# Kernel tuning notes

Measured on AMD Instinct MI355X. Metric: run time of the kernel, lower is better.

Reference implementation:

```python
import jax, jax.numpy as jnp
import numpy as np

# Config: 4 sparse batch items, each with 2048 active voxels (uniform-length case
# of sparse full self-attention). channels=1024, heads=16, head_dim=64.
B_SEQ, L, H, D = 4, 2048, 16, 64
C = H * D  # 1024
N = B_SEQ * L  # 8192
EPS = 1e-12  # F.normalize eps


def setup_inputs() -> dict:
    key = jax.random.key(0)
    ks = jax.random.split(key, 6)
    s = 1.0 / np.sqrt(C)
    return {
        "x": jax.random.normal(ks[0], (N, C), dtype=jnp.float32),
        "W_qkv": jax.random.normal(ks[1], (C, 3 * C), dtype=jnp.float32) * s,
        "b_qkv": jnp.zeros((3 * C,), dtype=jnp.float32),
        "gamma_q": jnp.ones((H, D), dtype=jnp.float32),
        "gamma_k": jnp.ones((H, D), dtype=jnp.float32),
        "W_out": jax.random.normal(ks[2], (C, C), dtype=jnp.float32) * s,
        "b_out": jnp.zeros((C,), dtype=jnp.float32),
    }


def _qk_rms_norm(t, gamma):
    # SparseMultiHeadRMSNorm: L2-normalize last dim, scale by gamma[h,d] * sqrt(D)
    norm = jnp.maximum(jnp.linalg.norm(t, axis=-1, keepdims=True), EPS)
    return (t / norm) * gamma * (D ** 0.5)


def reference(x, W_qkv, b_qkv, gamma_q, gamma_k, W_out, b_out):
    qkv = x @ W_qkv + b_qkv                       # [N, 3C]
    qkv = qkv.reshape(B_SEQ, L, 3, H, D)          # fused pre-reshape
    q, k, v = qkv[:, :, 0], qkv[:, :, 1], qkv[:, :, 2]  # [B,L,H,D]
    q = _qk_rms_norm(q, gamma_q)
    k = _qk_rms_norm(k, gamma_k)
    # full scaled dot-product attention within each sparse batch item
    scores = jnp.einsum('blhd,bmhd->bhlm', q, k) / (D ** 0.5)
    attn = jax.nn.softmax(scores, axis=-1)
    h = jnp.einsum('bhlm,bmhd->blhd', attn, v)    # [B,L,H,D]
    h = h.reshape(N, C)
    return h @ W_out + b_out
```

## Files before the change

kernel.cpp:

```cpp
#include <hip/hip_runtime.h>

using u16 = unsigned short;

typedef float  f32x4  __attribute__((ext_vector_type(4)));
typedef float  f32x16 __attribute__((ext_vector_type(16)));
typedef __bf16 bf16x8 __attribute__((ext_vector_type(8)));
typedef short  s16x8  __attribute__((ext_vector_type(8)));

#define DEVI __device__ __forceinline__

constexpr int TOK = 8192;
constexpr int CIN = 1024;
constexpr int C3  = 3072;
constexpr int NH  = 16;
constexpr int HD  = 64;
constexpr int SL  = 2048;
constexpr int BH  = 64;

constexpr float LOG2E = 1.4426950408889634f;

DEVI u16 f2bf(float x) {
  unsigned u = __builtin_bit_cast(unsigned, x);
  u += 0x7FFFu + ((u >> 16) & 1u);
  return (u16)(u >> 16);
}

DEVI f32x4 mfma16(s16x8 a, s16x8 b, f32x4 c) {
  return __builtin_amdgcn_mfma_f32_16x16x32_bf16(
      __builtin_bit_cast(bf16x8, a), __builtin_bit_cast(bf16x8, b), c, 0, 0, 0);
}

DEVI f32x16 mfma32(s16x8 a, s16x8 b, f32x16 c) {
  return __builtin_amdgcn_mfma_f32_32x32x16_bf16(
      __builtin_bit_cast(bf16x8, a), __builtin_bit_cast(bf16x8, b), c, 0, 0, 0);
}

DEVI void gload_lds16(const void* g, void* l) {
  __builtin_amdgcn_global_load_lds(
      (const __attribute__((address_space(1))) unsigned int*)g,
      (__attribute__((address_space(3))) unsigned int*)l, 16, 0, 0);
}

DEVI unsigned cvtpk(float lo, float hi) {
  unsigned r;
  asm("v_cvt_pk_bf16_f32 %0, %1, %2" : "=v"(r) : "v"(lo), "v"(hi));
  return r;
}

DEVI void plswap(unsigned& a, unsigned& b) {
  asm("v_permlane32_swap_b32 %0, %1" : "+v"(a), "+v"(b));
}

__global__ __launch_bounds__(256) void k_cvt_x(const float* __restrict__ x,
                                               u16* __restrict__ xb) {
  const int total = TOK * CIN / 4;
  for (int i = blockIdx.x * 256 + threadIdx.x; i < total; i += gridDim.x * 256) {
    float4 v = ((const float4*)x)[i];
    ushort4 o;
    o.x = f2bf(v.x); o.y = f2bf(v.y); o.z = f2bf(v.z); o.w = f2bf(v.w);
    ((ushort4*)xb)[i] = o;
  }
}

__global__ __launch_bounds__(256) void k_transpose(const float* __restrict__ in,
                                                   u16* __restrict__ out,
                                                   int R, int C) {
  __shared__ u16 t[64][72];
  int rt = R >> 6;
  int tr = (blockIdx.x % rt) << 6;
  int tc = (blockIdx.x / rt) << 6;
  int tid = threadIdx.x;
#pragma unroll
  for (int k2 = 0; k2 < 16; k2++) {
    int idx = k2 * 256 + tid;
    int r = idx >> 6, c = idx & 63;
    t[r][c] = f2bf(in[(size_t)(tr + r) * C + tc + c]);
  }
  __syncthreads();
#pragma unroll
  for (int k2 = 0; k2 < 16; k2++) {
    int idx = k2 * 256 + tid;
    int r = idx >> 6, c = idx & 63;
    out[(size_t)(tc + r) * R + tr + c] = t[c][r];
  }
}

__global__ __launch_bounds__(256) void k_bound(const float* __restrict__ gq,
                                               const float* __restrict__ gk,
                                               float* __restrict__ bnd) {
  const int tid = threadIdx.x;
  const int h = tid >> 4, s = tid & 15;
  float mv = 0.f;
#pragma unroll
  for (int j = 0; j < 4; j++) {
    int d = s * 4 + j;
    mv = fmaxf(mv, fabsf(gq[h * 64 + d] * gk[h * 64 + d]));
  }
  mv = fmaxf(mv, __shfl_xor(mv, 1));
  mv = fmaxf(mv, __shfl_xor(mv, 2));
  mv = fmaxf(mv, __shfl_xor(mv, 4));
  mv = fmaxf(mv, __shfl_xor(mv, 8));
  if (s == 0) bnd[h] = 8.0f * LOG2E * mv;
}

#define STAGE4(SLOT, KT)                                                 \
  { char* Ld = L + (SLOT) * 16384;                                       \
    const size_t ko = (size_t)(KT) * 64;              \
    gload_lds16(Ag + ko,          Ld + wq);                              \
    gload_lds16(Ag + ko + 131072, Ld + 4096 + wq);                       \
    gload_lds16(Bg + ko,          Ld + 8192 + wq);                       \
    gload_lds16(Bg + ko + 131072, Ld + 12288 + wq); }

#define KBODY32(KT, DOSTAGE, VMSTR)                                      \
  {                                                                      \
    if (DOSTAGE) STAGE4(((KT) + 2) % 3, (KT) + 2)                        \
    asm volatile("s_waitcnt " VMSTR ::: "memory");                       \
    __builtin_amdgcn_s_barrier();                                        \
    const char* Lb = L + ((KT) % 3) * 16384;                             \
    s16x8 af[4], bfr[4];                                                 \
    _Pragma("unroll")                                                    \
    for (int mf = 0; mf < 4; mf++)                                       \
      af[mf] = *(const s16x8*)(Lb + (wr + mf * 16 + l15) * 64 + g * 16); \
    _Pragma("unroll")                                                    \
    for (int nf = 0; nf < 4; nf++)                                       \
      bfr[nf] = *(const s16x8*)(Lb + 8192 + (wc + nf * 16 + l15) * 64 + g * 16); \
    __builtin_amdgcn_s_setprio(1);                                       \
    _Pragma("unroll")                                                    \
    for (int mf = 0; mf < 4; mf++)                                       \
      _Pragma("unroll")                                                  \
      for (int nf = 0; nf < 4; nf++)                                     \
        acc[mf][nf] = mfma16(af[mf], bfr[nf], acc[mf][nf]);              \
    __builtin_amdgcn_s_setprio(0);                                       \
    __builtin_amdgcn_s_barrier();                                        \
  }

DEVI void gemm_mainloop(const char* Ag, const char* Bg, char* L, int wq,
                        int wr, int wc, int l15, int g, f32x4 (&acc)[4][4]) {
  STAGE4(0, 0)
  STAGE4(1, 1)
#pragma unroll
  for (int kt = 0; kt < 30; ++kt) KBODY32(kt, 1, "vmcnt(8)")
  KBODY32(30, 0, "vmcnt(4)")
  KBODY32(31, 0, "vmcnt(0)")
}

__global__ __launch_bounds__(256, 3) void k_gemm_qkv(
    const u16* __restrict__ A, const u16* __restrict__ Bt,
    const float* __restrict__ bias, const float* __restrict__ gq,
    const float* __restrict__ gk,
    u16* __restrict__ Qn, u16* __restrict__ Kn, u16* __restrict__ Vt) {
  __shared__ __align__(16) char Lsh[3][16384];
  int bid = blockIdx.x;
  bid = (bid & 7) * 192 + (bid >> 3);
  const int bm = (bid / 24) * 128, bn = (bid % 24) * 128;
  const int tid = threadIdx.x, lane = tid & 63, w = tid >> 6;
  const int l15 = lane & 15, g = lane >> 4;
  const int wr = (w >> 1) * 64, wc = (w & 1) * 64;

  const int srow = tid >> 2, scol = (tid & 3) * 16;
  const char* Ag = (const char*)A + (size_t)(bm + srow) * 2048 + scol;
  const char* Bg = (const char*)Bt + (size_t)(bn + srow) * 2048 + scol;
  const int wq = w << 10;

  f32x4 acc[4][4];
#pragma unroll
  for (int i = 0; i < 4; i++)
#pragma unroll
    for (int j = 0; j < 4; j++) acc[i][j] = f32x4{0.f, 0.f, 0.f, 0.f};

  gemm_mainloop(Ag, Bg, (char*)Lsh, wq, wr, wc, l15, g, acc);

  const int c0 = bn + wc;
  const int sec = c0 >> 10;
  const int head = (c0 & 1023) >> 6;
  float bv[4], gv[4];
#pragma unroll
  for (int nf = 0; nf < 4; nf++) {
    bv[nf] = bias[c0 + nf * 16 + l15];
    gv[nf] = 1.f;
    if (sec == 0) gv[nf] = gq[head * 64 + nf * 16 + l15];
    if (sec == 1) gv[nf] = gk[head * 64 + nf * 16 + l15];
  }
#pragma unroll
  for (int mf = 0; mf < 4; mf++) {
#pragma unroll
    for (int nf = 0; nf < 4; nf++)
#pragma unroll
      for (int r = 0; r < 4; r++) acc[mf][nf][r] += bv[nf];
    if (sec < 2) {
#pragma unroll
      for (int r = 0; r < 4; r++) {
        float ss = 0.f;
#pragma unroll
        for (int nf = 0; nf < 4; nf++) ss += acc[mf][nf][r] * acc[mf][nf][r];
        ss += __shfl_xor(ss, 1); ss += __shfl_xor(ss, 2);
        ss += __shfl_xor(ss, 4); ss += __shfl_xor(ss, 8);
        float nrm = fmaxf(sqrtf(ss), 1e-12f);
        float f = (sec == 0 ? LOG2E : 8.0f) / nrm;
#pragma unroll
        for (int nf = 0; nf < 4; nf++) acc[mf][nf][r] *= f;
      }
    }
    int rbase = bm + wr + mf * 16 + 4 * g;
#pragma unroll
    for (int r = 0; r < 4; r++) {
      int row = rbase + r;
      int b = row >> 11, tok = row & 2047;
      int bh = b * NH + head;
#pragma unroll
      for (int nf = 0; nf < 4; nf++) {
        int d = nf * 16 + l15;
        u16 val = f2bf(acc[mf][nf][r] * gv[nf]);
        if (sec == 0)      Qn[((size_t)bh * SL + tok) * HD + d] = val;
        else if (sec == 1) Kn[((size_t)bh * SL + tok) * HD + d] = val;
        else               Vt[((size_t)bh * HD + d) * SL + tok] = val;
      }
    }
  }
}

__global__ __launch_bounds__(256, 3) void k_gemm_out(
    const u16* __restrict__ A, const u16* __restrict__ Bt,
    const float* __restrict__ bias, float* __restrict__ out) {
  __shared__ __align__(16) char Lsh[3][16384];
  int bid = blockIdx.x;
  bid = (bid & 7) * 64 + (bid >> 3);
  const int bm = (bid / 8) * 128, bn = (bid % 8) * 128;
  const int tid = threadIdx.x, lane = tid & 63, w = tid >> 6;
  const int l15 = lane & 15, g = lane >> 4;
  const int wr = (w >> 1) * 64, wc = (w & 1) * 64;

  const int srow = tid >> 2, scol = (tid & 3) * 16;
  const char* Ag = (const char*)A + (size_t)(bm + srow) * 2048 + scol;
  const char* Bg = (const char*)Bt + (size_t)(bn + srow) * 2048 + scol;
  const int wq = w << 10;

  f32x4 acc[4][4];
#pragma unroll
  for (int i = 0; i < 4; i++)
#pragma unroll
    for (int j = 0; j < 4; j++) acc[i][j] = f32x4{0.f, 0.f, 0.f, 0.f};

  gemm_mainloop(Ag, Bg, (char*)Lsh, wq, wr, wc, l15, g, acc);

  float bv[4];
#pragma unroll
  for (int nf = 0; nf < 4; nf++) bv[nf] = bias[bn + wc + nf * 16 + l15];
#pragma unroll
  for (int mf = 0; mf < 4; mf++)
#pragma unroll
    for (int r = 0; r < 4; r++) {
      int row = bm + wr + mf * 16 + 4 * g + r;
#pragma unroll
      for (int nf = 0; nf < 4; nf++)
        out[(size_t)row * CIN + bn + wc + nf * 16 + l15] = acc[mf][nf][r] + bv[nf];
    }
}

__global__ __launch_bounds__(512) void k_attn(const u16* __restrict__ Qn,
                                              const u16* __restrict__ Kn,
                                              const u16* __restrict__ Vt,
                                              const float* __restrict__ bnd,
                                              u16* __restrict__ hm) {
  __shared__ __align__(16) char KL[2][8192];
  __shared__ __align__(16) char VL[2][8192];
  const int bh = blockIdx.x & 63, qb = blockIdx.x >> 6;
  const int tid = threadIdx.x, w = tid >> 6, lane = tid & 63;
  const int l31 = lane & 31, h = lane >> 5;
  const int qr0 = qb * 256 + w * 32;
  const float negM = -bnd[bh & 15];

  const int sr  = tid >> 3;
  const int scb = ((tid & 7) << 4) ^ ((sr & 7) << 4);
  const char* kst = (const char*)(Kn + (size_t)bh * SL * HD) + (size_t)sr * 128 + scb;
  const char* vst = (const char*)(Vt + (size_t)bh * HD * SL) + (size_t)sr * 4096 + scb;
  char* kl0 = KL[0] + (w << 10);
  char* vl0 = VL[0] + (w << 10);
  char* kl1 = KL[1] + (w << 10);
  char* vl1 = VL[1] + (w << 10);

  const u16* Qb = Qn + ((size_t)bh * SL + qr0 + l31) * HD + 8 * h;
  s16x8 qf[4];
#pragma unroll
  for (int ks = 0; ks < 4; ks++) qf[ks] = *(const s16x8*)(Qb + ks * 16);

  const int lb = l31 * 128 + ((h << 4) ^ ((l31 & 7) << 4));

  f32x16 o0, o1;
#pragma unroll
  for (int i = 0; i < 16; i++) { o0[i] = 0.f; o1[i] = 0.f; }
  float lr = 0.f;

  gload_lds16(kst, kl0);
  gload_lds16(vst, vl0);
  __syncthreads();

  for (int it = 0; it < 32; ++it) {
    const char* KB = (it & 1) ? KL[1] : KL[0];
    const char* VB = (it & 1) ? VL[1] : VL[0];
    if (it < 31) {
      const size_t ko = (size_t)(it + 1) << 13;
      const size_t vo = (size_t)(it + 1) << 7;
      gload_lds16(kst + ko, (it & 1) ? kl0 : kl1);
      gload_lds16(vst + vo, (it & 1) ? vl0 : vl1);
    }

    f32x16 s0, s1;
#pragma unroll
    for (int i = 0; i < 16; i++) { s0[i] = negM; s1[i] = negM; }
    __builtin_amdgcn_s_setprio(1);
#pragma unroll
    for (int ks = 0; ks < 4; ks++) {
      const s16x8 ka  = *(const s16x8*)(KB + (lb ^ (ks << 5)));
      const s16x8 kb2 = *(const s16x8*)(KB + 4096 + (lb ^ (ks << 5)));
      s0 = mfma32(ka, qf[ks], s0);
      s1 = mfma32(kb2, qf[ks], s1);
    }
    __builtin_amdgcn_s_setprio(0);

#pragma unroll
    for (int i = 0; i < 16; i++) s0[i] = __builtin_amdgcn_exp2f(s0[i]);
#pragma unroll
    for (int i = 0; i < 16; i++) s1[i] = __builtin_amdgcn_exp2f(s1[i]);
    float sm8[8];
#pragma unroll
    for (int i = 0; i < 8; i++)
      sm8[i] = (s0[i] + s0[i + 8]) + (s1[i] + s1[i + 8]);
    lr += ((sm8[0] + sm8[1]) + (sm8[2] + sm8[3])) +
          ((sm8[4] + sm8[5]) + (sm8[6] + sm8[7]));

    union PBu { unsigned u[4]; s16x8 v; } pb;
#define MK_PB(SV, B)                              \
    {                                             \
      unsigned a0 = cvtpk(SV[B + 0], SV[B + 1]);  \
      unsigned c0 = cvtpk(SV[B + 4], SV[B + 5]);  \
      plswap(a0, c0);                             \
      unsigned a1 = cvtpk(SV[B + 2], SV[B + 3]);  \
      unsigned c1 = cvtpk(SV[B + 6], SV[B + 7]);  \
      plswap(a1, c1);                             \
      pb.u[0] = a0; pb.u[1] = a1; pb.u[2] = c0; pb.u[3] = c1; \
    }
#define PV_STEP(KS)                                            \
    {                                                          \
      const s16x8 va = *(const s16x8*)(VB + (lb ^ (KS << 5))); \
      const s16x8 vb = *(const s16x8*)(VB + 4096 + (lb ^ (KS << 5))); \
      __builtin_amdgcn_s_setprio(1);                           \
      o0 = mfma32(va, pb.v, o0);                               \
      o1 = mfma32(vb, pb.v, o1);                               \
      __builtin_amdgcn_s_setprio(0);                           \
    }
    MK_PB(s0, 0) PV_STEP(0)
    MK_PB(s0, 8) PV_STEP(1)
    MK_PB(s1, 0) PV_STEP(2)
    MK_PB(s1, 8) PV_STEP(3)
#undef MK_PB
#undef PV_STEP

    __syncthreads();
  }

  const float ltot = lr + __shfl_xor(lr, 32);
  const float inv = 1.f / ltot;
  const int bq = bh >> 4, hh = bh & 15;
  u16* hb = hm + ((size_t)bq * SL + qr0 + l31) * CIN + hh * HD;
#pragma unroll
  for (int rg = 0; rg < 4; rg++) {
    const int d0 = 8 * rg + 4 * h;
    unsigned lo = cvtpk(o0[4 * rg + 0] * inv, o0[4 * rg + 1] * inv);
    unsigned hi = cvtpk(o0[4 * rg + 2] * inv, o0[4 * rg + 3] * inv);
    *(unsigned long long*)(hb + d0) =
        (unsigned long long)lo | ((unsigned long long)hi << 32);
    unsigned lo1 = cvtpk(o1[4 * rg + 0] * inv, o1[4 * rg + 1] * inv);
    unsigned hi1 = cvtpk(o1[4 * rg + 2] * inv, o1[4 * rg + 3] * inv);
    *(unsigned long long*)(hb + 32 + d0) =
        (unsigned long long)lo1 | ((unsigned long long)hi1 << 32);
  }
}

extern "C" void kernel_launch(void* const* d_in, const int* in_sizes, int n_in,
                              void* d_out, int out_size, void* d_ws, size_t ws_size,
                              hipStream_t stream) {
  const float* x    = (const float*)d_in[0];
  const float* Wqkv = (const float*)d_in[1];
  const float* bqkv = (const float*)d_in[2];
  const float* gq   = (const float*)d_in[3];
  const float* gk   = (const float*)d_in[4];
  const float* Wout = (const float*)d_in[5];
  const float* bout = (const float*)d_in[6];
  float* out = (float*)d_out;

  char* ws = (char*)d_ws;
  u16* xb  = (u16*)(ws);
  u16* wqT = (u16*)(ws + 16777216);
  u16* woT = (u16*)(ws + 23068672);
  u16* Qn  = (u16*)(ws + 25165824);
  u16* Kn  = (u16*)(ws + 41943040);
  u16* Vt  = (u16*)(ws + 58720256);
  u16* hm  = (u16*)(ws + 75497472);
  float* bnd = (float*)xb;

  k_cvt_x<<<2048, 256, 0, stream>>>(x, xb);
  k_transpose<<<(1024 / 64) * (3072 / 64), 256, 0, stream>>>(Wqkv, wqT, 1024, 3072);
  k_transpose<<<(1024 / 64) * (1024 / 64), 256, 0, stream>>>(Wout, woT, 1024, 1024);
  k_gemm_qkv<<<(TOK / 128) * (C3 / 128), 256, 0, stream>>>(xb, wqT, bqkv, gq, gk, Qn, Kn, Vt);
  k_bound<<<1, 256, 0, stream>>>(gq, gk, bnd);
  k_attn<<<BH * (SL / 256), 512, 0, stream>>>(Qn, Kn, Vt, bnd, hm);
  k_gemm_out<<<(TOK / 128) * (CIN / 128), 256, 0, stream>>>(hm, woT, bout, out);
}
```

Before: 208.8 us.

## Merge prep kernels into one launch and double-buffer GEMM LDS for occupancy

Folds the x conversion, both weight transposes and the softmax bound computation into a single k_prep launch, so three kernel launches and their gaps go away. The bound buffer moves to its own workspace slot because xb is now written concurrently. The GEMM mainloops go from triple- to double-buffered LDS staging (prefetch depth one), which lowers LDS per block, and launch bounds are raised from 3 to 5 blocks per SM. The trade is less latency hiding per block in exchange for more resident blocks.

```diff
diff --git a/kernel.cpp b/kernel.cpp
--- a/kernel.cpp
+++ b/kernel.cpp
@@ -51,25 +51,11 @@
   asm("v_permlane32_swap_b32 %0, %1" : "+v"(a), "+v"(b));
 }
 
-__global__ __launch_bounds__(256) void k_cvt_x(const float* __restrict__ x,
-                                               u16* __restrict__ xb) {
-  const int total = TOK * CIN / 4;
-  for (int i = blockIdx.x * 256 + threadIdx.x; i < total; i += gridDim.x * 256) {
-    float4 v = ((const float4*)x)[i];
-    ushort4 o;
-    o.x = f2bf(v.x); o.y = f2bf(v.y); o.z = f2bf(v.z); o.w = f2bf(v.w);
-    ((ushort4*)xb)[i] = o;
-  }
-}
-
-__global__ __launch_bounds__(256) void k_transpose(const float* __restrict__ in,
-                                                   u16* __restrict__ out,
-                                                   int R, int C) {
-  __shared__ u16 t[64][72];
+DEVI void do_transpose(const float* __restrict__ in, u16* __restrict__ out,
+                       int R, int C, int blk, int tid, u16 (*t)[72]) {
   int rt = R >> 6;
-  int tr = (blockIdx.x % rt) << 6;
-  int tc = (blockIdx.x / rt) << 6;
-  int tid = threadIdx.x;
+  int tr = (blk % rt) << 6;
+  int tc = (blk / rt) << 6;
 #pragma unroll
   for (int k2 = 0; k2 < 16; k2++) {
     int idx = k2 * 256 + tid;
@@ -85,22 +71,40 @@
   }
 }
 
-__global__ __launch_bounds__(256) void k_bound(const float* __restrict__ gq,
-                                               const float* __restrict__ gk,
-                                               float* __restrict__ bnd) {
-  const int tid = threadIdx.x;
-  const int h = tid >> 4, s = tid & 15;
-  float mv = 0.f;
-#pragma unroll
-  for (int j = 0; j < 4; j++) {
-    int d = s * 4 + j;
-    mv = fmaxf(mv, fabsf(gq[h * 64 + d] * gk[h * 64 + d]));
-  }
-  mv = fmaxf(mv, __shfl_xor(mv, 1));
-  mv = fmaxf(mv, __shfl_xor(mv, 2));
-  mv = fmaxf(mv, __shfl_xor(mv, 4));
-  mv = fmaxf(mv, __shfl_xor(mv, 8));
-  if (s == 0) bnd[h] = 8.0f * LOG2E * mv;
+__global__ __launch_bounds__(256) void k_prep(
+    const float* __restrict__ x, u16* __restrict__ xb,
+    const float* __restrict__ Wqkv, u16* __restrict__ wqT,
+    const float* __restrict__ Wout, u16* __restrict__ woT,
+    const float* __restrict__ gq, const float* __restrict__ gk,
+    float* __restrict__ bnd) {
+  __shared__ u16 t[64][72];
+  const int bid = blockIdx.x, tid = threadIdx.x;
+  if (bid < 1024) {
+    const int total = TOK * CIN / 4;
+    for (int i = bid * 256 + tid; i < total; i += 1024 * 256) {
+      float4 v = ((const float4*)x)[i];
+      ushort4 o;
+      o.x = f2bf(v.x); o.y = f2bf(v.y); o.z = f2bf(v.z); o.w = f2bf(v.w);
+      ((ushort4*)xb)[i] = o;
+    }
+  } else if (bid < 1024 + 768) {
+    do_transpose(Wqkv, wqT, 1024, 3072, bid - 1024, tid, t);
+  } else if (bid < 1024 + 768 + 256) {
+    do_transpose(Wout, woT, 1024, 1024, bid - 1792, tid, t);
+  } else {
+    const int h = tid >> 4, s = tid & 15;
+    float mv = 0.f;
+#pragma unroll
+    for (int j = 0; j < 4; j++) {
+      int d = s * 4 + j;
+      mv = fmaxf(mv, fabsf(gq[h * 64 + d] * gk[h * 64 + d]));
+    }
+    mv = fmaxf(mv, __shfl_xor(mv, 1));
+    mv = fmaxf(mv, __shfl_xor(mv, 2));
+    mv = fmaxf(mv, __shfl_xor(mv, 4));
+    mv = fmaxf(mv, __shfl_xor(mv, 8));
+    if (s == 0) bnd[h] = 8.0f * LOG2E * mv;
+  }
 }
 
 #define STAGE4(SLOT, KT)                                                 \
@@ -111,12 +115,12 @@
     gload_lds16(Bg + ko,          Ld + 8192 + wq);                       \
     gload_lds16(Bg + ko + 131072, Ld + 12288 + wq); }
 
-#define KBODY32(KT, DOSTAGE, VMSTR)                                      \
+#define KBODY2(KT, DOSTAGE, VMSTR)                                       \
   {                                                                      \
-    if (DOSTAGE) STAGE4(((KT) + 2) % 3, (KT) + 2)                        \
+    if (DOSTAGE) STAGE4(((KT) + 1) & 1, (KT) + 1)                        \
     asm volatile("s_waitcnt " VMSTR ::: "memory");                       \
     __builtin_amdgcn_s_barrier();                                        \
-    const char* Lb = L + ((KT) % 3) * 16384;                             \
+    const char* Lb = L + ((KT) & 1) * 16384;                             \
     s16x8 af[4], bfr[4];                                                 \
     _Pragma("unroll")                                                    \
     for (int mf = 0; mf < 4; mf++)                                       \
@@ -137,19 +141,17 @@
 DEVI void gemm_mainloop(const char* Ag, const char* Bg, char* L, int wq,
                         int wr, int wc, int l15, int g, f32x4 (&acc)[4][4]) {
   STAGE4(0, 0)
-  STAGE4(1, 1)
-#pragma unroll
-  for (int kt = 0; kt < 30; ++kt) KBODY32(kt, 1, "vmcnt(8)")
-  KBODY32(30, 0, "vmcnt(4)")
-  KBODY32(31, 0, "vmcnt(0)")
-}
-
-__global__ __launch_bounds__(256, 3) void k_gemm_qkv(
+#pragma unroll
+  for (int kt = 0; kt < 31; ++kt) KBODY2(kt, 1, "vmcnt(4)")
+  KBODY2(31, 0, "vmcnt(0)")
+}
+
+__global__ __launch_bounds__(256, 5) void k_gemm_qkv(
     const u16* __restrict__ A, const u16* __restrict__ Bt,
     const float* __restrict__ bias, const float* __restrict__ gq,
     const float* __restrict__ gk,
     u16* __restrict__ Qn, u16* __restrict__ Kn, u16* __restrict__ Vt) {
-  __shared__ __align__(16) char Lsh[3][16384];
+  __shared__ __align__(16) char Lsh[2][16384];
   int bid = blockIdx.x;
   bid = (bid & 7) * 192 + (bid >> 3);
   const int bm = (bid / 24) * 128, bn = (bid % 24) * 128;
@@ -219,10 +221,10 @@
   }
 }
 
-__global__ __launch_bounds__(256, 3) void k_gemm_out(
+__global__ __launch_bounds__(256, 5) void k_gemm_out(
     const u16* __restrict__ A, const u16* __restrict__ Bt,
     const float* __restrict__ bias, float* __restrict__ out) {
-  __shared__ __align__(16) char Lsh[3][16384];
+  __shared__ __align__(16) char Lsh[2][16384];
   int bid = blockIdx.x;
   bid = (bid & 7) * 64 + (bid >> 3);
   const int bm = (bid / 8) * 128, bn = (bid % 8) * 128;
@@ -397,13 +399,10 @@
   u16* Kn  = (u16*)(ws + 41943040);
   u16* Vt  = (u16*)(ws + 58720256);
   u16* hm  = (u16*)(ws + 75497472);
-  float* bnd = (float*)xb;
-
-  k_cvt_x<<<2048, 256, 0, stream>>>(x, xb);
-  k_transpose<<<(1024 / 64) * (3072 / 64), 256, 0, stream>>>(Wqkv, wqT, 1024, 3072);
-  k_transpose<<<(1024 / 64) * (1024 / 64), 256, 0, stream>>>(Wout, woT, 1024, 1024);
+  float* bnd = (float*)(ws + 92274688);
+
+  k_prep<<<2049, 256, 0, stream>>>(x, xb, Wqkv, wqT, Wout, woT, gq, gk, bnd);
   k_gemm_qkv<<<(TOK / 128) * (C3 / 128), 256, 0, stream>>>(xb, wqT, bqkv, gq, gk, Qn, Kn, Vt);
-  k_bound<<<1, 256, 0, stream>>>(gq, gk, bnd);
   k_attn<<<BH * (SL / 256), 512, 0, stream>>>(Qn, Kn, Vt, bnd, hm);
   k_gemm_out<<<(TOK / 128) * (CIN / 128), 256, 0, stream>>>(hm, woT, bout, out);
 }
```

New measurement: 389.1 us. +86.4%, slower.
